# Kernel optimization log

Hardware: AMD Instinct MI355X
Metric: run time of the kernel (lower is better)

The kernel has to match this reference:

```python
import jax, jax.numpy as jnp
import numpy as np

N_NODES = 50000
N_EDGES = 800000
IN_DIM, HID_DIM, OUT_DIM = 64, 128, 128


def _glorot(key, shape):
    fan_in, fan_out = shape[1], shape[0]
    lim = float(np.sqrt(6.0 / (fan_in + fan_out)))
    return jax.random.uniform(key, shape, jnp.float32, -lim, lim)


def setup_inputs() -> dict:
    key = jax.random.key(0)
    ks = jax.random.split(key, 8)
    x = jax.random.normal(ks[0], (N_NODES, IN_DIM), jnp.float32)
    edge_index = jax.random.randint(ks[1], (2, N_EDGES), 0, N_NODES, jnp.int64)
    return {
        "x": x,
        "edge_index": edge_index,
        # layer 1 (SAGEConv: lin_l acts on aggregated neighbors + bias, lin_r on root)
        "W1_l": _glorot(ks[2], (HID_DIM, IN_DIM)),
        "W1_r": _glorot(ks[3], (HID_DIM, IN_DIM)),
        "b1": jnp.zeros((HID_DIM,), jnp.float32),
        # layer 2
        "W2_l": _glorot(ks[4], (OUT_DIM, HID_DIM)),
        "W2_r": _glorot(ks[5], (OUT_DIM, HID_DIM)),
        "b2": jnp.zeros((OUT_DIM,), jnp.float32),
    }


def _sage_conv(x, src, dst, W_l, W_r, b):
    # mean aggregation of neighbor features: messages flow src -> dst
    msg = x[src]                                           # [E, D]
    agg = jax.ops.segment_sum(msg, dst, num_segments=N_NODES)  # [N, D]
    deg = jax.ops.segment_sum(jnp.ones((msg.shape[0],), x.dtype), dst,
                              num_segments=N_NODES)        # [N]
    mean = agg / jnp.maximum(deg, 1.0)[:, None]            # isolated nodes -> 0
    return mean @ W_l.T + x @ W_r.T + b


def reference(x, edge_index, W1_l, W1_r, b1, W2_l, W2_r, b2):
    src, dst = edge_index[0], edge_index[1]
    h = _sage_conv(x, src, dst, W1_l, W1_r, b1)
    h = jax.nn.relu(h)
    out = _sage_conv(h, src, dst, W2_l, W2_r, b2)
    return out
```

## Files before the change

kernel.cpp:

```cpp
#include <hip/hip_runtime.h>
#include <hip/hip_bf16.h>

constexpr int N  = 50000;
constexpr int E  = 800000;
constexpr int D0 = 64;
constexpr int D1 = 128;
constexpr int CAP = 64;

constexpr int NPART = 8;
constexpr int PSZ   = (N + NPART - 1) / NPART;
constexpr int BPP   = 128;

typedef __attribute__((ext_vector_type(8))) short short8;
typedef __attribute__((ext_vector_type(4))) float f32x4;

__device__ __forceinline__ unsigned short bf16bits(float f) {
    __hip_bfloat16 hb = __float2bfloat16(f);
    return *reinterpret_cast<unsigned short*>(&hb);
}

__device__ __forceinline__ void acc8(float* a, const uint4 r) {
    union { unsigned u; float f; } c;
    c.u = r.x << 16;         a[0] += c.f;
    c.u = r.x & 0xffff0000u; a[1] += c.f;
    c.u = r.y << 16;         a[2] += c.f;
    c.u = r.y & 0xffff0000u; a[3] += c.f;
    c.u = r.z << 16;         a[4] += c.f;
    c.u = r.z & 0xffff0000u; a[5] += c.f;
    c.u = r.w << 16;         a[6] += c.f;
    c.u = r.w & 0xffff0000u; a[7] += c.f;
}

__global__ __launch_bounds__(256)
void k_bin(const int* __restrict__ src, const int* __restrict__ dst,
           int* __restrict__ cnt, int* __restrict__ bin) {
    const int p     = blockIdx.x & (NPART - 1);
    const int local = blockIdx.x >> 3;
    const int lo = p * PSZ;
    const int hi = min(N, lo + PSZ);

    for (int i = local * 256 + threadIdx.x; i < E / 4; i += BPP * 256) {
        const int e0 = i * 4;
        int4 d = *(const int4*)&dst[e0];
        int4 s = *(const int4*)&src[e0];
        if (d.x >= lo && d.x < hi) {
            int pos = atomicAdd(&cnt[d.x], 1);
            if (pos < CAP) bin[d.x * CAP + pos] = s.x;
        }
        if (d.y >= lo && d.y < hi) {
            int pos = atomicAdd(&cnt[d.y], 1);
            if (pos < CAP) bin[d.y * CAP + pos] = s.y;
        }
        if (d.z >= lo && d.z < hi) {
            int pos = atomicAdd(&cnt[d.z], 1);
            if (pos < CAP) bin[d.z * CAP + pos] = s.z;
        }
        if (d.w >= lo && d.w < hi) {
            int pos = atomicAdd(&cnt[d.w], 1);
            if (pos < CAP) bin[d.w * CAP + pos] = s.w;
        }
    }
}

__global__ void k_cvtx(const float* __restrict__ x, unsigned short* __restrict__ xb) {
    int i = blockIdx.x * blockDim.x + threadIdx.x;
    if (i >= N * D0 / 8) return;
    const float4 v0 = *(const float4*)&x[(size_t)i * 8];
    const float4 v1 = *(const float4*)&x[(size_t)i * 8 + 4];
    float f[8] = {v0.x, v0.y, v0.z, v0.w, v1.x, v1.y, v1.z, v1.w};
    unsigned short u[8];
    #pragma unroll
    for (int j = 0; j < 8; ++j) u[j] = bf16bits(f[j]);
    *(short8*)&xb[(size_t)i * 8] = *(short8*)u;
}

__global__ void k_wprep(const float* __restrict__ W1l, const float* __restrict__ W1r,
                        const float* __restrict__ W2l, const float* __restrict__ W2r,
                        unsigned short* __restrict__ W1cat,
                        unsigned short* __restrict__ W2cat) {
    int i = blockIdx.x * blockDim.x + threadIdx.x;
    if (i < 128 * 128) {
        int o = i >> 7, k = i & 127;
        float v = (k < 64) ? W1l[o * 64 + k] : W1r[o * 64 + (k - 64)];
        W1cat[i] = bf16bits(v);
    }
    if (i < 128 * 256) {
        int o = i >> 8, k = i & 255;
        float v = (k < 128) ? W2l[o * 128 + k] : W2r[o * 128 + (k - 128)];
        W2cat[i] = bf16bits(v);
    }
}

template<int DIN>
__global__ __launch_bounds__(256, 8)
void k_gather(const unsigned short* __restrict__ xin,
              const int* __restrict__ cnt,
              const int* __restrict__ bin,
              unsigned short* __restrict__ mean) {
    constexpr int GRPSZ = DIN / 8;
    constexpr int GPB   = 256 / GRPSZ;
    const int tid      = threadIdx.x;
    const int sub      = tid & (GRPSZ - 1);
    const int gloc     = tid / GRPSZ;
    const int lane     = tid & 63;
    const int lanebase = (lane / GRPSZ) * GRPSZ;
    const int g0   = blockIdx.x * GPB + gloc;
    const int gstr = gridDim.x * GPB;

    for (int n = g0; n < N; n += gstr) {
        const int deg  = cnt[n];
        const int degc = min(deg, CAP);
        const int base = n * CAP;

        float a[8] = {0.f, 0.f, 0.f, 0.f, 0.f, 0.f, 0.f, 0.f};

        for (int b = 0; b < degc; b += GRPSZ) {
            int nb = (b + sub < degc) ? bin[base + b + sub] : 0;
            const int c = min(GRPSZ, degc - b);
            int j = 0;
            for (; j + 4 <= c; j += 4) {
                int s0 = __shfl(nb, lanebase + j + 0);
                int s1 = __shfl(nb, lanebase + j + 1);
                int s2 = __shfl(nb, lanebase + j + 2);
                int s3 = __shfl(nb, lanebase + j + 3);
                uint4 r0 = *(const uint4*)&xin[(size_t)s0 * DIN + sub * 8];
                uint4 r1 = *(const uint4*)&xin[(size_t)s1 * DIN + sub * 8];
                uint4 r2 = *(const uint4*)&xin[(size_t)s2 * DIN + sub * 8];
                uint4 r3 = *(const uint4*)&xin[(size_t)s3 * DIN + sub * 8];
                acc8(a, r0); acc8(a, r1); acc8(a, r2); acc8(a, r3);
            }
            for (; j < c; ++j) {
                int s = __shfl(nb, lanebase + j);
                uint4 r = *(const uint4*)&xin[(size_t)s * DIN + sub * 8];
                acc8(a, r);
            }
        }

        const float invd = 1.0f / fmaxf((float)deg, 1.0f);
        unsigned short u[8];
        #pragma unroll
        for (int q = 0; q < 8; ++q) u[q] = bf16bits(a[q] * invd);
        *(short8*)&mean[(size_t)n * DIN + sub * 8] = *(short8*)u;
    }
}

template<int DIN, bool RELU, bool OUT_BF16>
__global__ __launch_bounds__(256)
void k_mdense(const unsigned short* __restrict__ mean,
              const unsigned short* __restrict__ xin,
              const unsigned short* __restrict__ Wcat,
              const float* __restrict__ bias,
              void* __restrict__ out,
              int n_nodes) {
    constexpr int K  = 2 * DIN;
    constexpr int KP = K + 8;
    __shared__ unsigned short A[64 * KP];

    const int tid   = threadIdx.x;
    const int nbase = blockIdx.x * 64;

    constexpr int CPR   = K / 8;
    constexpr int TOTAL = 64 * CPR;
    for (int c = tid; c < TOTAL; c += 256) {
        int row  = c / CPR;
        int col8 = (c - row * CPR) * 8;
        int n    = nbase + row;
        short8 v = (short8)0;
        if (n < n_nodes) {
            const unsigned short* srcp = (col8 < DIN)
                ? &mean[(size_t)n * DIN + col8]
                : &xin[(size_t)n * DIN + (col8 - DIN)];
            v = *(const short8*)srcp;
        }
        *(short8*)&A[row * KP + col8] = v;
    }
    __syncthreads();

    const int lane = tid & 63;
    const int wv   = tid >> 6;
    const int l15  = lane & 15;
    const int kseg = lane >> 4;

    f32x4 acc[8];
    #pragma unroll
    for (int ot = 0; ot < 8; ++ot) acc[ot] = (f32x4){0.f, 0.f, 0.f, 0.f};

    #pragma unroll
    for (int kk = 0; kk < K / 32; ++kk) {
        short8 a = *(const short8*)&A[(wv * 16 + l15) * KP + kk * 32 + kseg * 8];
        #pragma unroll
        for (int ot = 0; ot < 8; ++ot) {
            short8 b = *(const short8*)&Wcat[(size_t)(ot * 16 + l15) * K + kk * 32 + kseg * 8];
            acc[ot] = __builtin_amdgcn_mfma_f32_16x16x32_bf16(a, b, acc[ot], 0, 0, 0);
        }
    }

    #pragma unroll
    for (int ot = 0; ot < 8; ++ot) {
        const int o  = ot * 16 + l15;
        const float bv = bias[o];
        #pragma unroll
        for (int i = 0; i < 4; ++i) {
            int n = nbase + wv * 16 + kseg * 4 + i;
            if (n < n_nodes) {
                float v = acc[ot][i] + bv;
                if constexpr (RELU) v = fmaxf(v, 0.0f);
                if constexpr (OUT_BF16) {
                    ((unsigned short*)out)[(size_t)n * 128 + o] = bf16bits(v);
                } else {
                    ((float*)out)[(size_t)n * 128 + o] = v;
                }
            }
        }
    }
}

extern "C" void kernel_launch(void* const* d_in, const int* in_sizes, int n_in,
                              void* d_out, int out_size, void* d_ws, size_t ws_size,
                              hipStream_t stream) {
    const float* x   = (const float*)d_in[0];
    const int*   ei  = (const int*)d_in[1];
    const float* W1l = (const float*)d_in[2];
    const float* W1r = (const float*)d_in[3];
    const float* b1  = (const float*)d_in[4];
    const float* W2l = (const float*)d_in[5];
    const float* W2r = (const float*)d_in[6];
    const float* b2  = (const float*)d_in[7];
    float*       out = (float*)d_out;

    const int* src = ei;
    const int* dst = ei + E;

    char* p = (char*)d_ws;
    auto alloc = [&](size_t bytes) -> char* {
        char* r = p; p += (bytes + 15) & ~(size_t)15; return r;
    };
    int*            cnt   = (int*)alloc(N * sizeof(int));
    int*            bin   = (int*)alloc((size_t)N * CAP * sizeof(int));
    unsigned short* xb    = (unsigned short*)alloc((size_t)N * D0 * 2);
    unsigned short* h     = (unsigned short*)alloc((size_t)N * D1 * 2);
    unsigned short* mean  = (unsigned short*)alloc((size_t)N * D1 * 2);
    unsigned short* W1cat = (unsigned short*)alloc(128 * 128 * 2);
    unsigned short* W2cat = (unsigned short*)alloc(128 * 256 * 2);

    const int nblk_d = (N + 63) / 64;

    k_cvtx<<<(N * D0 / 8 + 255) / 256, 256, 0, stream>>>(x, xb);
    k_wprep<<<(128 * 256 + 255) / 256, 256, 0, stream>>>(W1l, W1r, W2l, W2r, W1cat, W2cat);

    hipMemsetAsync(cnt, 0, (size_t)N * sizeof(int), stream);
    k_bin<<<NPART * BPP, 256, 0, stream>>>(src, dst, cnt, bin);

    k_gather<D0><<<2048, 256, 0, stream>>>(xb, cnt, bin, mean);
    k_mdense<D0, true, true>
        <<<nblk_d, 256, 0, stream>>>(mean, xb, W1cat, b1, h, N);

    k_gather<D1><<<2048, 256, 0, stream>>>(h, cnt, bin, mean);
    k_mdense<D1, false, false>
        <<<nblk_d, 256, 0, stream>>>(mean, h, W2cat, b2, out, N);
}
```

Measured before the change: 173.1 us.

## Fuse prep kernels with count reset, store bins as u16, unroll gather by 8

```diff
diff --git a/kernel.cpp b/kernel.cpp
--- a/kernel.cpp
+++ b/kernel.cpp
@@ -32,8 +32,37 @@
 }
 
 __global__ __launch_bounds__(256)
+void k_prep(const float* __restrict__ x, unsigned short* __restrict__ xb,
+            const float* __restrict__ W1l, const float* __restrict__ W1r,
+            const float* __restrict__ W2l, const float* __restrict__ W2r,
+            unsigned short* __restrict__ W1cat, unsigned short* __restrict__ W2cat,
+            int* __restrict__ cnt) {
+    int i = blockIdx.x * blockDim.x + threadIdx.x;
+    if (i < N / 4) ((int4*)cnt)[i] = make_int4(0, 0, 0, 0);
+    if (i < 128 * 128) {
+        int o = i >> 7, k = i & 127;
+        float v = (k < 64) ? W1l[o * 64 + k] : W1r[o * 64 + (k - 64)];
+        W1cat[i] = bf16bits(v);
+    }
+    if (i < 128 * 256) {
+        int o = i >> 8, k = i & 255;
+        float v = (k < 128) ? W2l[o * 128 + k] : W2r[o * 128 + (k - 128)];
+        W2cat[i] = bf16bits(v);
+    }
+    if (i < N * D0 / 8) {
+        const float4 v0 = *(const float4*)&x[(size_t)i * 8];
+        const float4 v1 = *(const float4*)&x[(size_t)i * 8 + 4];
+        float f[8] = {v0.x, v0.y, v0.z, v0.w, v1.x, v1.y, v1.z, v1.w};
+        unsigned short u[8];
+        #pragma unroll
+        for (int j = 0; j < 8; ++j) u[j] = bf16bits(f[j]);
+        *(short8*)&xb[(size_t)i * 8] = *(short8*)u;
+    }
+}
+
+__global__ __launch_bounds__(256)
 void k_bin(const int* __restrict__ src, const int* __restrict__ dst,
-           int* __restrict__ cnt, int* __restrict__ bin) {
+           int* __restrict__ cnt, unsigned short* __restrict__ bin) {
     const int p     = blockIdx.x & (NPART - 1);
     const int local = blockIdx.x >> 3;
     const int lo = p * PSZ;
@@ -45,49 +74,20 @@
         int4 s = *(const int4*)&src[e0];
         if (d.x >= lo && d.x < hi) {
             int pos = atomicAdd(&cnt[d.x], 1);
-            if (pos < CAP) bin[d.x * CAP + pos] = s.x;
+            if (pos < CAP) bin[(size_t)d.x * CAP + pos] = (unsigned short)s.x;
         }
         if (d.y >= lo && d.y < hi) {
             int pos = atomicAdd(&cnt[d.y], 1);
-            if (pos < CAP) bin[d.y * CAP + pos] = s.y;
+            if (pos < CAP) bin[(size_t)d.y * CAP + pos] = (unsigned short)s.y;
         }
         if (d.z >= lo && d.z < hi) {
             int pos = atomicAdd(&cnt[d.z], 1);
-            if (pos < CAP) bin[d.z * CAP + pos] = s.z;
+            if (pos < CAP) bin[(size_t)d.z * CAP + pos] = (unsigned short)s.z;
         }
         if (d.w >= lo && d.w < hi) {
             int pos = atomicAdd(&cnt[d.w], 1);
-            if (pos < CAP) bin[d.w * CAP + pos] = s.w;
-        }
-    }
-}
-
-__global__ void k_cvtx(const float* __restrict__ x, unsigned short* __restrict__ xb) {
-    int i = blockIdx.x * blockDim.x + threadIdx.x;
-    if (i >= N * D0 / 8) return;
-    const float4 v0 = *(const float4*)&x[(size_t)i * 8];
-    const float4 v1 = *(const float4*)&x[(size_t)i * 8 + 4];
-    float f[8] = {v0.x, v0.y, v0.z, v0.w, v1.x, v1.y, v1.z, v1.w};
-    unsigned short u[8];
-    #pragma unroll
-    for (int j = 0; j < 8; ++j) u[j] = bf16bits(f[j]);
-    *(short8*)&xb[(size_t)i * 8] = *(short8*)u;
-}
-
-__global__ void k_wprep(const float* __restrict__ W1l, const float* __restrict__ W1r,
-                        const float* __restrict__ W2l, const float* __restrict__ W2r,
-                        unsigned short* __restrict__ W1cat,
-                        unsigned short* __restrict__ W2cat) {
-    int i = blockIdx.x * blockDim.x + threadIdx.x;
-    if (i < 128 * 128) {
-        int o = i >> 7, k = i & 127;
-        float v = (k < 64) ? W1l[o * 64 + k] : W1r[o * 64 + (k - 64)];
-        W1cat[i] = bf16bits(v);
-    }
-    if (i < 128 * 256) {
-        int o = i >> 8, k = i & 255;
-        float v = (k < 128) ? W2l[o * 128 + k] : W2r[o * 128 + (k - 128)];
-        W2cat[i] = bf16bits(v);
+            if (pos < CAP) bin[(size_t)d.w * CAP + pos] = (unsigned short)s.w;
+        }
     }
 }
 
@@ -95,7 +95,7 @@
 __global__ __launch_bounds__(256, 8)
 void k_gather(const unsigned short* __restrict__ xin,
               const int* __restrict__ cnt,
-              const int* __restrict__ bin,
+              const unsigned short* __restrict__ bin,
               unsigned short* __restrict__ mean) {
     constexpr int GRPSZ = DIN / 8;
     constexpr int GPB   = 256 / GRPSZ;
@@ -110,14 +110,34 @@
     for (int n = g0; n < N; n += gstr) {
         const int deg  = cnt[n];
         const int degc = min(deg, CAP);
-        const int base = n * CAP;
+        const size_t base = (size_t)n * CAP;
 
         float a[8] = {0.f, 0.f, 0.f, 0.f, 0.f, 0.f, 0.f, 0.f};
 
         for (int b = 0; b < degc; b += GRPSZ) {
-            int nb = (b + sub < degc) ? bin[base + b + sub] : 0;
+            int nb = (b + sub < degc) ? (int)bin[base + b + sub] : 0;
             const int c = min(GRPSZ, degc - b);
             int j = 0;
+            for (; j + 8 <= c; j += 8) {
+                int s0 = __shfl(nb, lanebase + j + 0);
+                int s1 = __shfl(nb, lanebase + j + 1);
+                int s2 = __shfl(nb, lanebase + j + 2);
+                int s3 = __shfl(nb, lanebase + j + 3);
+                int s4 = __shfl(nb, lanebase + j + 4);
+                int s5 = __shfl(nb, lanebase + j + 5);
+                int s6 = __shfl(nb, lanebase + j + 6);
+                int s7 = __shfl(nb, lanebase + j + 7);
+                uint4 r0 = *(const uint4*)&xin[(size_t)s0 * DIN + sub * 8];
+                uint4 r1 = *(const uint4*)&xin[(size_t)s1 * DIN + sub * 8];
+                uint4 r2 = *(const uint4*)&xin[(size_t)s2 * DIN + sub * 8];
+                uint4 r3 = *(const uint4*)&xin[(size_t)s3 * DIN + sub * 8];
+                uint4 r4 = *(const uint4*)&xin[(size_t)s4 * DIN + sub * 8];
+                uint4 r5 = *(const uint4*)&xin[(size_t)s5 * DIN + sub * 8];
+                uint4 r6 = *(const uint4*)&xin[(size_t)s6 * DIN + sub * 8];
+                uint4 r7 = *(const uint4*)&xin[(size_t)s7 * DIN + sub * 8];
+                acc8(a, r0); acc8(a, r1); acc8(a, r2); acc8(a, r3);
+                acc8(a, r4); acc8(a, r5); acc8(a, r6); acc8(a, r7);
+            }
             for (; j + 4 <= c; j += 4) {
                 int s0 = __shfl(nb, lanebase + j + 0);
                 int s1 = __shfl(nb, lanebase + j + 1);
@@ -236,7 +256,7 @@
         char* r = p; p += (bytes + 15) & ~(size_t)15; return r;
     };
     int*            cnt   = (int*)alloc(N * sizeof(int));
-    int*            bin   = (int*)alloc((size_t)N * CAP * sizeof(int));
+    unsigned short* bin   = (unsigned short*)alloc((size_t)N * CAP * 2);
     unsigned short* xb    = (unsigned short*)alloc((size_t)N * D0 * 2);
     unsigned short* h     = (unsigned short*)alloc((size_t)N * D1 * 2);
     unsigned short* mean  = (unsigned short*)alloc((size_t)N * D1 * 2);
@@ -245,10 +265,9 @@
 
     const int nblk_d = (N + 63) / 64;
 
-    k_cvtx<<<(N * D0 / 8 + 255) / 256, 256, 0, stream>>>(x, xb);
-    k_wprep<<<(128 * 256 + 255) / 256, 256, 0, stream>>>(W1l, W1r, W2l, W2r, W1cat, W2cat);
-
-    hipMemsetAsync(cnt, 0, (size_t)N * sizeof(int), stream);
+    k_prep<<<(N * D0 / 8 + 255) / 256, 256, 0, stream>>>(
+        x, xb, W1l, W1r, W2l, W2r, W1cat, W2cat, cnt);
+
     k_bin<<<NPART * BPP, 256, 0, stream>>>(src, dst, cnt, bin);
 
     k_gather<D0><<<2048, 256, 0, stream>>>(xb, cnt, bin, mean);
```

After: 250.8 us. +44.9%, slower.
